# Performance work log

Hardware: AMD Instinct MI355X
Metric: run time of the kernel (lower is better)

The kernel has to match this reference:

```python
import jax, jax.numpy as jnp
import numpy as np

N_NODES = 10000
N_EDGES = 640000
IN_CH = 128
HID = 256
OUT_CH = 10
NUM_GRAPHS = 64
EPS = 0.0  # non-trainable buffer, initial_eps=0


def setup_inputs() -> dict:
    key = jax.random.key(0)
    ks = jax.random.split(key, 12)
    x = jax.random.normal(ks[0], (N_NODES, IN_CH), dtype=jnp.float32)
    edge_index = jax.random.randint(ks[1], (2, N_EDGES), 0, N_NODES, dtype=jnp.int64)
    batch = jnp.sort(jax.random.randint(ks[2], (N_NODES,), 0, NUM_GRAPHS, dtype=jnp.int64))
    edge_weights = jax.random.uniform(ks[3], (N_EDGES,), dtype=jnp.float32)
    def lin(k, fan_in, fan_out):
        bound = 1.0 / np.sqrt(fan_in)
        kw, kb = jax.random.split(k)
        W = jax.random.uniform(kw, (fan_out, fan_in), minval=-bound, maxval=bound, dtype=jnp.float32)
        b = jax.random.uniform(kb, (fan_out,), minval=-bound, maxval=bound, dtype=jnp.float32)
        return W, b
    W1, b1 = lin(ks[4], IN_CH, HID)
    W2, b2 = lin(ks[5], HID, HID)
    W3, b3 = lin(ks[6], HID, HID)
    Wl, bl = lin(ks[7], HID, OUT_CH)
    return {"x": x, "edge_index": edge_index, "batch": batch, "edge_weights": edge_weights,
            "W1": W1, "b1": b1, "W2": W2, "b2": b2, "W3": W3, "b3": b3, "Wl": Wl, "bl": bl}


def _ginw_conv(x, edge_index, edge_weights, W, b):
    # message: edge_weight * x_j (source nodes), aggregated by add at target i
    src, dst = edge_index[0], edge_index[1]
    msg = edge_weights[:, None] * x[src]           # [E, F]
    agg = jax.ops.segment_sum(msg, dst, num_segments=N_NODES)  # [N, F]
    out = agg + (1.0 + EPS) * x
    return out @ W.T + b


def reference(x, edge_index, batch, edge_weights, W1, b1, W2, b2, W3, b3, Wl, bl):
    h = jax.nn.relu(_ginw_conv(x, edge_index, edge_weights, W1, b1))
    h = jax.nn.relu(_ginw_conv(h, edge_index, edge_weights, W2, b2))
    h = jax.nn.relu(_ginw_conv(h, edge_index, edge_weights, W3, b3))
    # global mean pool over graphs
    sums = jax.ops.segment_sum(h, batch, num_segments=NUM_GRAPHS)        # [G, HID]
    cnts = jax.ops.segment_sum(jnp.ones((N_NODES,), h.dtype), batch, num_segments=NUM_GRAPHS)
    pooled = sums / jnp.maximum(cnts, 1.0)[:, None]
    return pooled @ Wl.T + bl
```

## Files before the change

kernel.cpp:

```cpp
#include <hip/hip_runtime.h>
#include <hip/hip_fp16.h>

namespace {
constexpr int NN   = 10000;
constexpr int NE   = 640000;
constexpr int INC  = 128;
constexpr int HIDC = 256;
constexpr int OUTC = 10;
constexpr int NG   = 64;
constexpr int DCAP = 128;
constexpr int SB   = 16;
constexpr int EPB  = NE / SB;
constexpr int CB   = 240;
}

typedef __attribute__((ext_vector_type(8))) _Float16 half8;
typedef __attribute__((ext_vector_type(4))) float f32x4;
typedef __attribute__((ext_vector_type(4))) ushort u16x4;

__device__ __forceinline__ ushort f2h(float f) { return __half_as_ushort(__float2half(f)); }
__device__ __forceinline__ float h2f(ushort u) { return __half2float(__ushort_as_half(u)); }

__global__ __launch_bounds__(256) void zero_kernel(int* __restrict__ deg,
                                                   float* __restrict__ pooled) {
    const int gt = blockIdx.x * 256 + threadIdx.x;
    const int gs = gridDim.x * 256;
    for (int i = gt; i < NN; i += gs) deg[i] = 0;
    for (int i = gt; i < NG * HIDC; i += gs) pooled[i] = 0.0f;
}

__global__ __launch_bounds__(1024) void build_kernel(const int* __restrict__ ei,
                                                     const float* __restrict__ ew,
                                                     int* __restrict__ deg,
                                                     uint* __restrict__ erec,
                                                     const float* __restrict__ x,
                                                     ushort* __restrict__ xh,
                                                     const float* __restrict__ W1,
                                                     ushort* __restrict__ w1h,
                                                     const float* __restrict__ W2,
                                                     ushort* __restrict__ w2h,
                                                     const float* __restrict__ W3,
                                                     ushort* __restrict__ w3h) {
    __shared__ int hist[NN];
    const int t = threadIdx.x;
    const int bid = blockIdx.x;

    if (bid < SB) {
        const int ebase = bid * EPB;
        for (int i = t; i < NN; i += 1024) hist[i] = 0;
        __syncthreads();

        for (int it = 0; it < 10; ++it) {
            const int vi = it * 4096 + t * 4;
            if (vi < EPB) {
                const int4 d4 = *(const int4*)(ei + NE + ebase + vi);
                atomicAdd(&hist[d4.x], 1);
                atomicAdd(&hist[d4.y], 1);
                atomicAdd(&hist[d4.z], 1);
                atomicAdd(&hist[d4.w], 1);
            }
        }
        __syncthreads();

        for (int b = t; b < NN; b += 1024) {
            const int c = hist[b];
            if (c > 0) hist[b] = atomicAdd(&deg[b], c);
        }
        __syncthreads();

        for (int it = 0; it < 10; ++it) {
            const int vi = it * 4096 + t * 4;
            if (vi < EPB) {
                const int e = ebase + vi;
                const int4 s4 = *(const int4*)(ei + e);
                const int4 d4 = *(const int4*)(ei + NE + e);
                const float4 w4 = *(const float4*)(ew + e);
                {
                    const int idx = atomicAdd(&hist[d4.x], 1);
                    if (idx < DCAP) erec[((size_t)d4.x << 7) + idx] = ((uint)s4.x << 16) | f2h(w4.x);
                }
                {
                    const int idx = atomicAdd(&hist[d4.y], 1);
                    if (idx < DCAP) erec[((size_t)d4.y << 7) + idx] = ((uint)s4.y << 16) | f2h(w4.y);
                }
                {
                    const int idx = atomicAdd(&hist[d4.z], 1);
                    if (idx < DCAP) erec[((size_t)d4.z << 7) + idx] = ((uint)s4.z << 16) | f2h(w4.z);
                }
                {
                    const int idx = atomicAdd(&hist[d4.w], 1);
                    if (idx < DCAP) erec[((size_t)d4.w << 7) + idx] = ((uint)s4.w << 16) | f2h(w4.w);
                }
            }
        }
        return;
    }

    const int gt = (bid - SB) * 1024 + t;
    const int gs = CB * 1024;
    {
        const int n4 = NN * INC / 4;
        for (int i = gt; i < n4; i += gs) {
            f32x4 v = __builtin_nontemporal_load((const f32x4*)x + i);
            u16x4 o;
#pragma unroll
            for (int j = 0; j < 4; j++) o[j] = f2h(v[j]);
            __builtin_nontemporal_store(o, (u16x4*)xh + i);
        }
    }
    {
        const int n4 = HIDC * INC / 4;
        for (int i = gt; i < n4; i += gs) {
            f32x4 v = __builtin_nontemporal_load((const f32x4*)W1 + i);
            u16x4 o;
#pragma unroll
            for (int j = 0; j < 4; j++) o[j] = f2h(v[j]);
            __builtin_nontemporal_store(o, (u16x4*)w1h + i);
        }
    }
    {
        const int n4 = HIDC * HIDC / 4;
        for (int i = gt; i < n4; i += gs) {
            f32x4 v = __builtin_nontemporal_load((const f32x4*)W2 + i);
            u16x4 o;
#pragma unroll
            for (int j = 0; j < 4; j++) o[j] = f2h(v[j]);
            __builtin_nontemporal_store(o, (u16x4*)w2h + i);
            f32x4 v3 = __builtin_nontemporal_load((const f32x4*)W3 + i);
            u16x4 o3;
#pragma unroll
            for (int j = 0; j < 4; j++) o3[j] = f2h(v3[j]);
            __builtin_nontemporal_store(o3, (u16x4*)w3h + i);
        }
    }
}

__global__ __launch_bounds__(256) void gather128_kernel(const int* __restrict__ deg,
                                                        const uint* __restrict__ erec,
                                                        const ushort* __restrict__ x,
                                                        ushort* __restrict__ out) {
    constexpr int U = 8;
    const int n = blockIdx.x * 4 + (threadIdx.x >> 6);
    if (n >= NN) return;
    const int lane = threadIdx.x & 63;
    const int sub = lane >> 5;
    const int cl  = lane & 31;
    const int d = min(deg[n], DCAP);
    const int beg = n << 7;
    const size_t loff = (size_t)cl * 4;
    const ushort* xr = x + loff;

    float a0, a1, a2, a3;
    {
        u16x4 v = *(const u16x4*)(x + (size_t)n * INC + loff);
        a0 = sub ? 0.f : h2f(v[0]);
        a1 = sub ? 0.f : h2f(v[1]);
        a2 = sub ? 0.f : h2f(v[2]);
        a3 = sub ? 0.f : h2f(v[3]);
    }

    int e = 0;
    for (; e + 2 * U <= d; e += 2 * U) {
        uint rec[U];
#pragma unroll
        for (int u = 0; u < U; u++) rec[u] = erec[beg + e + 2 * u + sub];
        u16x4 v[U];
#pragma unroll
        for (int u = 0; u < U; u++)
            v[u] = *(const u16x4*)(xr + (size_t)(rec[u] >> 16) * INC);
#pragma unroll
        for (int u = 0; u < U; u++) {
            const float w = h2f((ushort)(rec[u] & 0xFFFFu));
            a0 += w * h2f(v[u][0]);
            a1 += w * h2f(v[u][1]);
            a2 += w * h2f(v[u][2]);
            a3 += w * h2f(v[u][3]);
        }
    }
    for (; e + 2 <= d; e += 2) {
        const uint rec = erec[beg + e + sub];
        const float w = h2f((ushort)(rec & 0xFFFFu));
        const u16x4 v = *(const u16x4*)(xr + (size_t)(rec >> 16) * INC);
        a0 += w * h2f(v[0]); a1 += w * h2f(v[1]); a2 += w * h2f(v[2]); a3 += w * h2f(v[3]);
    }
    if (e < d && sub == 0) {
        const uint rec = erec[beg + e];
        const float w = h2f((ushort)(rec & 0xFFFFu));
        const u16x4 v = *(const u16x4*)(xr + (size_t)(rec >> 16) * INC);
        a0 += w * h2f(v[0]); a1 += w * h2f(v[1]); a2 += w * h2f(v[2]); a3 += w * h2f(v[3]);
    }

    a0 += __shfl_xor(a0, 32, 64);
    a1 += __shfl_xor(a1, 32, 64);
    a2 += __shfl_xor(a2, 32, 64);
    a3 += __shfl_xor(a3, 32, 64);
    if (sub == 0) {
        u16x4 o;
        o[0] = f2h(a0); o[1] = f2h(a1); o[2] = f2h(a2); o[3] = f2h(a3);
        __builtin_nontemporal_store(o, (u16x4*)(out + (size_t)n * INC + loff));
    }
}

__global__ __launch_bounds__(256) void gather_half_kernel(const int* __restrict__ deg,
                                                          const uint* __restrict__ erec,
                                                          const ushort* __restrict__ x,
                                                          ushort* __restrict__ out) {
    constexpr int U = 8;
    const int half = blockIdx.x & 1;
    const int n = (blockIdx.x >> 1) * 4 + (threadIdx.x >> 6);
    if (n >= NN) return;
    const int lane = threadIdx.x & 63;
    const int sub = lane >> 5;
    const int cl  = lane & 31;
    const int d = min(deg[n], DCAP);
    const int beg = n << 7;
    const size_t loff = (size_t)half * 128 + cl * 4;
    const ushort* xr = x + loff;

    float a0, a1, a2, a3;
    {
        u16x4 v = *(const u16x4*)(x + (size_t)n * HIDC + loff);
        a0 = sub ? 0.f : h2f(v[0]);
        a1 = sub ? 0.f : h2f(v[1]);
        a2 = sub ? 0.f : h2f(v[2]);
        a3 = sub ? 0.f : h2f(v[3]);
    }

    int e = 0;
    for (; e + 2 * U <= d; e += 2 * U) {
        uint rec[U];
#pragma unroll
        for (int u = 0; u < U; u++) rec[u] = erec[beg + e + 2 * u + sub];
        u16x4 v[U];
#pragma unroll
        for (int u = 0; u < U; u++)
            v[u] = *(const u16x4*)(xr + (size_t)(rec[u] >> 16) * HIDC);
#pragma unroll
        for (int u = 0; u < U; u++) {
            const float w = h2f((ushort)(rec[u] & 0xFFFFu));
            a0 += w * h2f(v[u][0]);
            a1 += w * h2f(v[u][1]);
            a2 += w * h2f(v[u][2]);
            a3 += w * h2f(v[u][3]);
        }
    }
    for (; e + 2 <= d; e += 2) {
        const uint rec = erec[beg + e + sub];
        const float w = h2f((ushort)(rec & 0xFFFFu));
        const u16x4 v = *(const u16x4*)(xr + (size_t)(rec >> 16) * HIDC);
        a0 += w * h2f(v[0]); a1 += w * h2f(v[1]); a2 += w * h2f(v[2]); a3 += w * h2f(v[3]);
    }
    if (e < d && sub == 0) {
        const uint rec = erec[beg + e];
        const float w = h2f((ushort)(rec & 0xFFFFu));
        const u16x4 v = *(const u16x4*)(xr + (size_t)(rec >> 16) * HIDC);
        a0 += w * h2f(v[0]); a1 += w * h2f(v[1]); a2 += w * h2f(v[2]); a3 += w * h2f(v[3]);
    }

    a0 += __shfl_xor(a0, 32, 64);
    a1 += __shfl_xor(a1, 32, 64);
    a2 += __shfl_xor(a2, 32, 64);
    a3 += __shfl_xor(a3, 32, 64);
    if (sub == 0) {
        u16x4 o;
        o[0] = f2h(a0); o[1] = f2h(a1); o[2] = f2h(a2); o[3] = f2h(a3);
        __builtin_nontemporal_store(o, (u16x4*)(out + (size_t)n * HIDC + loff));
    }
}

template <int K>
__global__ __launch_bounds__(256) void mfma_gemm_kernel(const ushort* __restrict__ A,
                                                        const ushort* __restrict__ Wb,
                                                        const float* __restrict__ bias,
                                                        ushort* __restrict__ C, int M) {
    constexpr int LDW = K + 8;
    __shared__ ushort Ws[64 * LDW];
    const int tid = threadIdx.x;
    const int bm = blockIdx.x * 128;
    const int bn = blockIdx.y * 64;

    constexpr int CPR = K / 8;
    for (int idx = tid; idx < 64 * CPR; idx += 256) {
        int r = idx / CPR, c = idx % CPR;
        uint4 v = *(const uint4*)(Wb + (size_t)(bn + r) * K + c * 8);
        *(uint4*)(&Ws[r * LDW + c * 8]) = v;
    }
    __syncthreads();

    const int wave = tid >> 6;
    const int lane = tid & 63;
    const int lrow = lane & 15;
    const int lq   = lane >> 4;
    const int m0 = bm + wave * 32;

    f32x4 acc[2][4] = {};
    const int r0 = min(m0 + lrow, M - 1);
    const int r1 = min(m0 + 16 + lrow, M - 1);

    for (int k0 = 0; k0 < K; k0 += 32) {
        const int kk = k0 + lq * 8;
        half8 a0 = __builtin_nontemporal_load((const half8*)(A + (size_t)r0 * K + kk));
        half8 a1 = __builtin_nontemporal_load((const half8*)(A + (size_t)r1 * K + kk));
        half8 b[4];
#pragma unroll
        for (int j = 0; j < 4; j++)
            b[j] = *(const half8*)(&Ws[(j * 16 + lrow) * LDW + kk]);
#pragma unroll
        for (int j = 0; j < 4; j++) {
            acc[0][j] = __builtin_amdgcn_mfma_f32_16x16x32_f16(a0, b[j], acc[0][j], 0, 0, 0);
            acc[1][j] = __builtin_amdgcn_mfma_f32_16x16x32_f16(a1, b[j], acc[1][j], 0, 0, 0);
        }
    }

#pragma unroll
    for (int sub = 0; sub < 2; sub++) {
#pragma unroll
        for (int j = 0; j < 4; j++) {
            const int gn = bn + j * 16 + lrow;
            const float bv = bias[gn];
#pragma unroll
            for (int i = 0; i < 4; i++) {
                const int gm = m0 + sub * 16 + lq * 4 + i;
                if (gm < M) {
                    float v = acc[sub][j][i] + bv;
                    v = fmaxf(v, 0.0f);
                    C[(size_t)gm * HIDC + gn] = f2h(v);
                }
            }
        }
    }
}

__global__ __launch_bounds__(256) void mfma_gemm_pool_kernel(const ushort* __restrict__ A,
                                                             const ushort* __restrict__ Wb,
                                                             const float* __restrict__ bias,
                                                             const int* __restrict__ batch,
                                                             float* __restrict__ pooled, int M) {
    constexpr int K = HIDC;
    constexpr int LDW = K + 8;
    __shared__ ushort Ws[64 * LDW];
    __shared__ float pl[6][64];
    const int tid = threadIdx.x;
    const int bm = blockIdx.x * 128;
    const int bn = blockIdx.y * 64;

    constexpr int CPR = K / 8;
    for (int idx = tid; idx < 64 * CPR; idx += 256) {
        int r = idx / CPR, c = idx % CPR;
        uint4 v = *(const uint4*)(Wb + (size_t)(bn + r) * K + c * 8);
        *(uint4*)(&Ws[r * LDW + c * 8]) = v;
    }
    for (int i = tid; i < 6 * 64; i += 256) pl[i >> 6][i & 63] = 0.0f;
    __syncthreads();

    const int wave = tid >> 6;
    const int lane = tid & 63;
    const int lrow = lane & 15;
    const int lq   = lane >> 4;
    const int m0 = bm + wave * 32;
    const int g0 = batch[bm];

    f32x4 acc[2][4] = {};
    const int r0 = min(m0 + lrow, M - 1);
    const int r1 = min(m0 + 16 + lrow, M - 1);

    for (int k0 = 0; k0 < K; k0 += 32) {
        const int kk = k0 + lq * 8;
        half8 a0 = __builtin_nontemporal_load((const half8*)(A + (size_t)r0 * K + kk));
        half8 a1 = __builtin_nontemporal_load((const half8*)(A + (size_t)r1 * K + kk));
        half8 b[4];
#pragma unroll
        for (int j = 0; j < 4; j++)
            b[j] = *(const half8*)(&Ws[(j * 16 + lrow) * LDW + kk]);
#pragma unroll
        for (int j = 0; j < 4; j++) {
            acc[0][j] = __builtin_amdgcn_mfma_f32_16x16x32_f16(a0, b[j], acc[0][j], 0, 0, 0);
            acc[1][j] = __builtin_amdgcn_mfma_f32_16x16x32_f16(a1, b[j], acc[1][j], 0, 0, 0);
        }
    }

#pragma unroll
    for (int sub = 0; sub < 2; sub++) {
#pragma unroll
        for (int i = 0; i < 4; i++) {
            const int gm = m0 + sub * 16 + lq * 4 + i;
            if (gm < M) {
                const int gi = min(batch[gm] - g0, 5);
#pragma unroll
                for (int j = 0; j < 4; j++) {
                    const int gn = bn + j * 16 + lrow;
                    float v = acc[sub][j][i] + bias[gn];
                    v = fmaxf(v, 0.0f);
                    atomicAdd(&pl[gi][j * 16 + lrow], v);
                }
            }
        }
    }
    __syncthreads();

    for (int i = tid; i < 6 * 64; i += 256) {
        const int s = i >> 6, col = i & 63;
        const float v = pl[s][col];
        const int gg = g0 + s;
        if (v != 0.0f && gg < NG)
            atomicAdd(&pooled[(size_t)gg * HIDC + bn + col], v);
    }
}

__device__ __forceinline__ int lower_bound_batch(const int* __restrict__ batch, int val) {
    int lo = 0, hi = NN;
    while (lo < hi) {
        int mid = (lo + hi) >> 1;
        if (batch[mid] < val) lo = mid + 1;
        else hi = mid;
    }
    return lo;
}

__global__ __launch_bounds__(256) void head_kernel(const float* __restrict__ pooled,
                                                   const int* __restrict__ batch,
                                                   const float* __restrict__ Wl,
                                                   const float* __restrict__ bl,
                                                   float* __restrict__ out) {
    __shared__ float s[HIDC];
    __shared__ float s2[OUTC][8];
    const int g = blockIdx.x;
    const int t = threadIdx.x;
    const int lo = lower_bound_batch(batch, g);
    const int hi = lower_bound_batch(batch, g + 1);
    const float inv = 1.0f / fmaxf((float)(hi - lo), 1.0f);
    if (t < HIDC) s[t] = pooled[(size_t)g * HIDC + t] * inv;
    __syncthreads();

    if (t < OUTC * 8) {
        const int oc = t >> 3, q = t & 7;
        float acc = 0.f;
        for (int k = q * 32; k < q * 32 + 32; k++)
            acc += s[k] * Wl[(size_t)oc * HIDC + k];
        s2[oc][q] = acc;
    }
    __syncthreads();
    if (t < OUTC) {
        float acc = bl[t];
#pragma unroll
        for (int q = 0; q < 8; q++) acc += s2[t][q];
        out[(size_t)g * OUTC + t] = acc;
    }
}

extern "C" void kernel_launch(void* const* d_in, const int* in_sizes, int n_in,
                              void* d_out, int out_size, void* d_ws, size_t ws_size,
                              hipStream_t stream) {
    const float* x     = (const float*)d_in[0];
    const int*   ei    = (const int*)d_in[1];
    const int*   batch = (const int*)d_in[2];
    const float* ew    = (const float*)d_in[3];
    const float* W1    = (const float*)d_in[4];
    const float* b1    = (const float*)d_in[5];
    const float* W2    = (const float*)d_in[6];
    const float* b2    = (const float*)d_in[7];
    const float* W3    = (const float*)d_in[8];
    const float* b3    = (const float*)d_in[9];
    const float* Wl    = (const float*)d_in[10];
    const float* bl    = (const float*)d_in[11];

    char* p = (char*)d_ws;
    ushort* xh     = (ushort*)p; p += (size_t)NN * INC * 2;
    ushort* agg128 = (ushort*)p; p += (size_t)NN * INC * 2;
    ushort* agg256 = (ushort*)p; p += (size_t)NN * HIDC * 2;
    ushort* h      = (ushort*)p; p += (size_t)NN * HIDC * 2;
    ushort* w1h    = (ushort*)p; p += (size_t)HIDC * INC * 2;
    ushort* w2h    = (ushort*)p; p += (size_t)HIDC * HIDC * 2;
    ushort* w3h    = (ushort*)p; p += (size_t)HIDC * HIDC * 2;
    uint*   erec   = (uint*)p;   p += (size_t)NN * DCAP * 4;
    int*    deg    = (int*)p;    p += (size_t)NN * 4;
    float*  pooled = (float*)p;  p += (size_t)NG * HIDC * 4;

    zero_kernel<<<32, 256, 0, stream>>>(deg, pooled);
    build_kernel<<<SB + CB, 1024, 0, stream>>>(ei, ew, deg, erec, x, xh,
                                               W1, w1h, W2, w2h, W3, w3h);

    const int gather_grid = (NN + 3) / 4;
    dim3 gemm_grid((NN + 127) / 128, HIDC / 64);

    gather128_kernel<<<gather_grid, 256, 0, stream>>>(deg, erec, xh, agg128);
    mfma_gemm_kernel<INC><<<gemm_grid, 256, 0, stream>>>(agg128, w1h, b1, h, NN);

    gather_half_kernel<<<gather_grid * 2, 256, 0, stream>>>(deg, erec, h, agg256);
    mfma_gemm_kernel<HIDC><<<gemm_grid, 256, 0, stream>>>(agg256, w2h, b2, h, NN);

    gather_half_kernel<<<gather_grid * 2, 256, 0, stream>>>(deg, erec, h, agg256);
    mfma_gemm_pool_kernel<<<gemm_grid, 256, 0, stream>>>(agg256, w3h, b3, batch, pooled, NN);

    head_kernel<<<NG, 256, 0, stream>>>(pooled, batch, Wl, bl, (float*)d_out);
}
```

Baseline: 265.4 us.

## Partition CSR build across node ranges and edge slices in all blocks

The edge bucketing moves from 16 dedicated blocks, each holding a full 10000-entry histogram, to all 256 blocks. Each block covers one of 8 destination-node ranges and one of 32 edge slices, with a 1250-entry LDS histogram. Every block then also does the fp16 conversion work. This spreads the atomic-heavy build across the whole GPU and shrinks LDS use, at the cost of each block reading its edge slice and discarding about 7/8 of the destinations.

Result: faster. 241.1 us (-9.2%).

```diff
diff --git a/kernel.cpp b/kernel.cpp
--- a/kernel.cpp
+++ b/kernel.cpp
@@ -9,9 +9,10 @@
 constexpr int OUTC = 10;
 constexpr int NG   = 64;
 constexpr int DCAP = 128;
-constexpr int SB   = 16;
-constexpr int EPB  = NE / SB;
-constexpr int CB   = 240;
+constexpr int NRG  = 8;
+constexpr int RNG  = NN / NRG;
+constexpr int SLICES = 32;
+constexpr int EPSL   = NE / SLICES;
 }
 
 typedef __attribute__((ext_vector_type(8))) _Float16 half8;
@@ -41,63 +42,61 @@
                                                      ushort* __restrict__ w2h,
                                                      const float* __restrict__ W3,
                                                      ushort* __restrict__ w3h) {
-    __shared__ int hist[NN];
+    __shared__ int hist[RNG];
     const int t = threadIdx.x;
-    const int bid = blockIdx.x;
-
-    if (bid < SB) {
-        const int ebase = bid * EPB;
-        for (int i = t; i < NN; i += 1024) hist[i] = 0;
-        __syncthreads();
-
-        for (int it = 0; it < 10; ++it) {
-            const int vi = it * 4096 + t * 4;
-            if (vi < EPB) {
-                const int4 d4 = *(const int4*)(ei + NE + ebase + vi);
-                atomicAdd(&hist[d4.x], 1);
-                atomicAdd(&hist[d4.y], 1);
-                atomicAdd(&hist[d4.z], 1);
-                atomicAdd(&hist[d4.w], 1);
-            }
-        }
-        __syncthreads();
-
-        for (int b = t; b < NN; b += 1024) {
-            const int c = hist[b];
-            if (c > 0) hist[b] = atomicAdd(&deg[b], c);
-        }
-        __syncthreads();
-
-        for (int it = 0; it < 10; ++it) {
-            const int vi = it * 4096 + t * 4;
-            if (vi < EPB) {
-                const int e = ebase + vi;
-                const int4 s4 = *(const int4*)(ei + e);
-                const int4 d4 = *(const int4*)(ei + NE + e);
-                const float4 w4 = *(const float4*)(ew + e);
-                {
-                    const int idx = atomicAdd(&hist[d4.x], 1);
-                    if (idx < DCAP) erec[((size_t)d4.x << 7) + idx] = ((uint)s4.x << 16) | f2h(w4.x);
-                }
-                {
-                    const int idx = atomicAdd(&hist[d4.y], 1);
-                    if (idx < DCAP) erec[((size_t)d4.y << 7) + idx] = ((uint)s4.y << 16) | f2h(w4.y);
-                }
-                {
-                    const int idx = atomicAdd(&hist[d4.z], 1);
-                    if (idx < DCAP) erec[((size_t)d4.z << 7) + idx] = ((uint)s4.z << 16) | f2h(w4.z);
-                }
-                {
-                    const int idx = atomicAdd(&hist[d4.w], 1);
-                    if (idx < DCAP) erec[((size_t)d4.w << 7) + idx] = ((uint)s4.w << 16) | f2h(w4.w);
-                }
-            }
-        }
-        return;
-    }
-
-    const int gt = (bid - SB) * 1024 + t;
-    const int gs = CB * 1024;
+    const int rx = blockIdx.x & (NRG - 1);
+    const int s  = blockIdx.x >> 3;
+    const int nlo = rx * RNG;
+    const int ebase = s * EPSL;
+
+    for (int i = t; i < RNG; i += 1024) hist[i] = 0;
+    __syncthreads();
+
+    for (int vi = t * 4; vi < EPSL; vi += 4096) {
+        const int4 d4 = *(const int4*)(ei + NE + ebase + vi);
+        int rl;
+        rl = d4.x - nlo; if ((uint)rl < (uint)RNG) atomicAdd(&hist[rl], 1);
+        rl = d4.y - nlo; if ((uint)rl < (uint)RNG) atomicAdd(&hist[rl], 1);
+        rl = d4.z - nlo; if ((uint)rl < (uint)RNG) atomicAdd(&hist[rl], 1);
+        rl = d4.w - nlo; if ((uint)rl < (uint)RNG) atomicAdd(&hist[rl], 1);
+    }
+    __syncthreads();
+
+    for (int b = t; b < RNG; b += 1024) {
+        const int c = hist[b];
+        if (c > 0) hist[b] = atomicAdd(&deg[nlo + b], c);
+    }
+    __syncthreads();
+
+    for (int vi = t * 4; vi < EPSL; vi += 4096) {
+        const int4 s4 = *(const int4*)(ei + ebase + vi);
+        const int4 d4 = *(const int4*)(ei + NE + ebase + vi);
+        const float4 w4 = *(const float4*)(ew + ebase + vi);
+        int rl;
+        rl = d4.x - nlo;
+        if ((uint)rl < (uint)RNG) {
+            const int idx = atomicAdd(&hist[rl], 1);
+            if (idx < DCAP) erec[((size_t)(nlo + rl) << 7) + idx] = ((uint)s4.x << 16) | f2h(w4.x);
+        }
+        rl = d4.y - nlo;
+        if ((uint)rl < (uint)RNG) {
+            const int idx = atomicAdd(&hist[rl], 1);
+            if (idx < DCAP) erec[((size_t)(nlo + rl) << 7) + idx] = ((uint)s4.y << 16) | f2h(w4.y);
+        }
+        rl = d4.z - nlo;
+        if ((uint)rl < (uint)RNG) {
+            const int idx = atomicAdd(&hist[rl], 1);
+            if (idx < DCAP) erec[((size_t)(nlo + rl) << 7) + idx] = ((uint)s4.z << 16) | f2h(w4.z);
+        }
+        rl = d4.w - nlo;
+        if ((uint)rl < (uint)RNG) {
+            const int idx = atomicAdd(&hist[rl], 1);
+            if (idx < DCAP) erec[((size_t)(nlo + rl) << 7) + idx] = ((uint)s4.w << 16) | f2h(w4.w);
+        }
+    }
+
+    const int gt = blockIdx.x * 1024 + t;
+    const int gs = 256 * 1024;
     {
         const int n4 = NN * INC / 4;
         for (int i = gt; i < n4; i += gs) {
@@ -477,8 +476,8 @@
     float*  pooled = (float*)p;  p += (size_t)NG * HIDC * 4;
 
     zero_kernel<<<32, 256, 0, stream>>>(deg, pooled);
-    build_kernel<<<SB + CB, 1024, 0, stream>>>(ei, ew, deg, erec, x, xh,
-                                               W1, w1h, W2, w2h, W3, w3h);
+    build_kernel<<<NRG * SLICES, 1024, 0, stream>>>(ei, ew, deg, erec, x, xh,
+                                                    W1, w1h, W2, w2h, W3, w3h);
 
     const int gather_grid = (NN + 3) / 4;
     dim3 gemm_grid((NN + 127) / 128, HIDC / 64);
```
